# Performance work log

Hardware: AMD Instinct MI355X
Metric: run time of the kernel (lower is better)

Reference implementation:

```python
import jax, jax.numpy as jnp
import numpy as np

K = 3        # kernel_size
PAD = 1      # padding
STRIDE = 1   # stride (must be 1: module asserts offset HxW == input HxW)
DIL = 1      # dilation


def _bilinear_gather(x, py, px):
    """x: (B,C,H,W); py,px: (B,KK,Ho,Wo) float sample coords.
    Returns (B,C,KK,Ho,Wo), zero outside bounds (DCNv2 semantics)."""
    B, C, H, W = x.shape
    y0 = jnp.floor(py); x0 = jnp.floor(px)
    wy1 = py - y0; wy0 = 1.0 - wy1
    wx1 = px - x0; wx0 = 1.0 - wx1
    flat = x.reshape(B, C, H * W)

    def gather(yi, xi):
        valid = (yi >= 0) & (yi < H) & (xi >= 0) & (xi < W)
        yc = jnp.clip(yi, 0, H - 1).astype(jnp.int32)
        xc = jnp.clip(xi, 0, W - 1).astype(jnp.int32)
        idx = (yc * W + xc).reshape(B, 1, -1)                      # (B,1,KK*Ho*Wo)
        g = jnp.take_along_axis(flat, jnp.broadcast_to(idx, (B, C, idx.shape[-1])), axis=2)
        g = g.reshape(B, C, *yi.shape[1:])                          # (B,C,KK,Ho,Wo)
        return jnp.where(valid[:, None], g, 0.0)

    v00 = gather(y0, x0)
    v01 = gather(y0, x0 + 1)
    v10 = gather(y0 + 1, x0)
    v11 = gather(y0 + 1, x0 + 1)
    wy0 = wy0[:, None]; wy1 = wy1[:, None]; wx0 = wx0[:, None]; wx1 = wx1[:, None]
    return wy0 * (wx0 * v00 + wx1 * v01) + wy1 * (wx0 * v10 + wx1 * v11)


def dcn_v2(x, coord_offset, coord_weight, weight, bias):
    B, C, H, W = x.shape
    O = weight.shape[0]
    KK = K * K
    # offset channels ordered (k, [y,x]) per DCNv2 layout
    offs = coord_offset.reshape(B, KK, 2, H, W)
    oy, ox = offs[:, :, 0], offs[:, :, 1]
    ky, kx = jnp.meshgrid(jnp.arange(K), jnp.arange(K), indexing='ij')
    ky = ky.reshape(KK); kx = kx.reshape(KK)
    # base sampling grid for each output pixel / kernel tap: (KK,H,W)
    py = (jnp.arange(H) * STRIDE - PAD)[None, :, None] + (ky * DIL)[:, None, None]
    px = (jnp.arange(W) * STRIDE - PAD)[None, None, :] + (kx * DIL)[:, None, None]
    py = py.astype(x.dtype)[None] + oy   # (B,KK,H,W)
    px = px.astype(x.dtype)[None] + ox
    sampled = _bilinear_gather(x, py, px)              # (B,C,KK,H,W)
    sampled = sampled * coord_weight[:, None]          # modulation mask
    out = jnp.einsum('bckhw,ock->bohw', sampled, weight.reshape(O, C, KK))
    return out + bias[None, :, None, None]


def setup_inputs() -> dict:
    key = jax.random.key(0)
    k1, k2, k3, k4, k5 = jax.random.split(key, 5)
    B, C, O, H, W = 8, 256, 256, 64, 64
    return {
        'input': jax.random.normal(k1, (B, C, H, W), dtype=jnp.float32),
        'coord_offset': jax.random.normal(k2, (B, 2 * K * K, H, W), dtype=jnp.float32),
        'coord_weight': jax.random.uniform(k3, (B, K * K, H, W), dtype=jnp.float32),
        'weight': jax.random.normal(k4, (O, C, K, K), dtype=jnp.float32) * 0.02,
        'bias': jax.random.normal(k5, (O,), dtype=jnp.float32) * 0.01,
    }


def reference(input, coord_offset, coord_weight, weight, bias):
    return dcn_v2(input, coord_offset, coord_weight, weight, bias)
```

## Files before the change

### kernel.cpp

```cpp
#include <hip/hip_runtime.h>
#include <hip/hip_bf16.h>
#include <stdint.h>

typedef __bf16 bf16_t;
typedef bf16_t bf16x8 __attribute__((ext_vector_type(8)));
typedef float f32x4 __attribute__((ext_vector_type(4)));
typedef float f32x2 __attribute__((ext_vector_type(2)));

__global__ __launch_bounds__(256) void k_transpose(const float* __restrict__ x,
                                                   bf16_t* __restrict__ xt) {
    __shared__ __align__(16) bf16_t tile[256][66];
    const int b = blockIdx.x >> 6;
    const int y = blockIdx.x & 63;
    const int t = threadIdx.x;

    const float* src = x + ((size_t)(b * 256) * 64 + y) * 64;
    const int x4 = (t & 15) * 4;
    const int cs = t >> 4;
#pragma unroll
    for (int cc = 0; cc < 256; cc += 16) {
        int c = cc + cs;
        float4 v = *(const float4*)(src + (size_t)c * 4096 + x4);
        tile[c][x4 + 0] = (bf16_t)v.x;
        tile[c][x4 + 1] = (bf16_t)v.y;
        tile[c][x4 + 2] = (bf16_t)v.z;
        tile[c][x4 + 3] = (bf16_t)v.w;
    }
    __syncthreads();
    bf16_t* dst = xt + ((size_t)(b * 64 + y) * 64) * 256 + t;
#pragma unroll 8
    for (int xx = 0; xx < 64; ++xx) {
        dst[(size_t)xx * 256] = tile[t][xx];
    }
}

__global__ __launch_bounds__(256) void k_pack_w(const float* __restrict__ w,
                                                bf16_t* __restrict__ Wp) {
    const int kb2 = blockIdx.x;
    const int kk  = kb2 >> 2;
    const int cp  = kb2 & 3;
    const int o   = threadIdx.x;
    bf16_t* base = Wp + (size_t)kb2 * 16384 + o * 64;
#pragma unroll
    for (int j = 0; j < 8; ++j) {
        const int js = j ^ (o & 7);
        bf16x8 v;
#pragma unroll
        for (int e = 0; e < 8; ++e) {
            const int c = cp * 64 + j * 8 + e;
            v[e] = (bf16_t)w[(size_t)(o * 256 + c) * 9 + kk];
        }
        *(bf16x8*)(base + js * 8) = v;
    }
}

__global__ __launch_bounds__(512, 4) void k_dcn(
    const bf16_t* __restrict__ xt, const bf16_t* __restrict__ Wp,
    const float* __restrict__ coff, const float* __restrict__ cwm,
    const float* __restrict__ bias, float* __restrict__ out) {

    __shared__ __align__(16) bf16_t sW[256 * 64];
    __shared__ __align__(16) bf16_t sS[64 * 64];
    __shared__ float sCW[4][64];
    __shared__ int   sCA[4][64];

    const int blk = blockIdx.x;
    const int b  = blk & 7;
    const int h  = blk >> 3;
    const int t = threadIdx.x;
    const int wv = t >> 6;
    const int lane = t & 63;

    const int p = t >> 3;
    const int q = t & 7;

    const int fr = lane & 15;
    const int quad = lane >> 4;
    const int swz = fr & 7;

    f32x4 acc[2][4] = {};

    for (int kk = 0; kk < 9; ++kk) {
        if (t < 64) {
            const int wpx = t;
            float oy = coff[((size_t)(b * 18 + kk * 2 + 0) * 64 + h) * 64 + wpx];
            float ox = coff[((size_t)(b * 18 + kk * 2 + 1) * 64 + h) * 64 + wpx];
            float m  = cwm [((size_t)(b * 9 + kk) * 64 + h) * 64 + wpx];
            float py = (float)(h - 1 + (kk / 3)) + oy;
            float px = (float)(wpx - 1 + (kk % 3)) + ox;
            float fy = floorf(py), fx = floorf(px);
            int y0 = (int)fy, x0 = (int)fx;
            int y1 = y0 + 1,  x1 = x0 + 1;
            float wy1 = py - fy, wx1 = px - fx;
            float wy0 = 1.0f - wy1, wx0 = 1.0f - wx1;
            bool vy0 = (y0 >= 0) && (y0 < 64), vy1 = (y1 >= 0) && (y1 < 64);
            bool vx0 = (x0 >= 0) && (x0 < 64), vx1 = (x1 >= 0) && (x1 < 64);
            int yc0 = min(max(y0, 0), 63), yc1 = min(max(y1, 0), 63);
            int xc0 = min(max(x0, 0), 63), xc1 = min(max(x1, 0), 63);
            const int base = b * 4096;
            sCW[0][wpx] = (vy0 && vx0) ? wy0 * wx0 * m : 0.0f;
            sCW[1][wpx] = (vy0 && vx1) ? wy0 * wx1 * m : 0.0f;
            sCW[2][wpx] = (vy1 && vx0) ? wy1 * wx0 * m : 0.0f;
            sCW[3][wpx] = (vy1 && vx1) ? wy1 * wx1 * m : 0.0f;
            sCA[0][wpx] = (base + yc0 * 64 + xc0) * 256;
            sCA[1][wpx] = (base + yc0 * 64 + xc1) * 256;
            sCA[2][wpx] = (base + yc1 * 64 + xc0) * 256;
            sCA[3][wpx] = (base + yc1 * 64 + xc1) * 256;
        }
        __syncthreads();

        const float w0 = sCW[0][p], w1 = sCW[1][p];
        const float w2 = sCW[2][p], w3 = sCW[3][p];
        const bf16_t* c0 = xt + sCA[0][p] + q * 8;
        const bf16_t* c1 = xt + sCA[1][p] + q * 8;
        const bf16_t* c2 = xt + sCA[2][p] + q * 8;
        const bf16_t* c3 = xt + sCA[3][p] + q * 8;
        bf16_t* sSp = sS + p * 64 + ((q ^ (p & 7)) * 8);

        for (int cp = 0; cp < 4; ++cp) {
            {
                const char* g = ((const char*)Wp)
                              + ((size_t)(kk * 4 + cp)) * 32768 + t * 16;
                char* l = ((char*)sW) + t * 16;
#pragma unroll
                for (int i = 0; i < 4; ++i) {
                    __builtin_amdgcn_global_load_lds(
                        (const __attribute__((address_space(1))) unsigned int*)(g + i * 8192),
                        (__attribute__((address_space(3))) unsigned int*)(l + i * 8192),
                        16, 0, 0);
                }
            }
            {
                const int cb = cp * 64;
                f32x2 s2[4] = {};
                {
                    bf16x8 v = *(const bf16x8*)(c0 + cb);
                    f32x2 ww = {w0, w0};
#pragma unroll
                    for (int j = 0; j < 4; ++j) { f32x2 f = {(float)v[2 * j], (float)v[2 * j + 1]}; s2[j] += ww * f; }
                }
                {
                    bf16x8 v = *(const bf16x8*)(c1 + cb);
                    f32x2 ww = {w1, w1};
#pragma unroll
                    for (int j = 0; j < 4; ++j) { f32x2 f = {(float)v[2 * j], (float)v[2 * j + 1]}; s2[j] += ww * f; }
                }
                {
                    bf16x8 v = *(const bf16x8*)(c2 + cb);
                    f32x2 ww = {w2, w2};
#pragma unroll
                    for (int j = 0; j < 4; ++j) { f32x2 f = {(float)v[2 * j], (float)v[2 * j + 1]}; s2[j] += ww * f; }
                }
                {
                    bf16x8 v = *(const bf16x8*)(c3 + cb);
                    f32x2 ww = {w3, w3};
#pragma unroll
                    for (int j = 0; j < 4; ++j) { f32x2 f = {(float)v[2 * j], (float)v[2 * j + 1]}; s2[j] += ww * f; }
                }
                bf16x8 ov;
#pragma unroll
                for (int j = 0; j < 4; ++j) {
                    ov[2 * j]     = (bf16_t)s2[j][0];
                    ov[2 * j + 1] = (bf16_t)s2[j][1];
                }
                *(bf16x8*)sSp = ov;
            }
            __syncthreads();

#pragma unroll
            for (int s = 0; s < 2; ++s) {
                const int cidx = s * 4 + quad;
                const int coff_e = (cidx ^ swz) * 8;
                bf16x8 a[2], bb[4];
#pragma unroll
                for (int mt = 0; mt < 2; ++mt)
                    a[mt] = *(const bf16x8*)(sW + (wv * 32 + mt * 16 + fr) * 64 + coff_e);
#pragma unroll
                for (int nt = 0; nt < 4; ++nt)
                    bb[nt] = *(const bf16x8*)(sS + (nt * 16 + fr) * 64 + coff_e);
#pragma unroll
                for (int mt = 0; mt < 2; ++mt)
#pragma unroll
                    for (int nt = 0; nt < 4; ++nt)
                        acc[mt][nt] = __builtin_amdgcn_mfma_f32_16x16x32_bf16(
                            a[mt], bb[nt], acc[mt][nt], 0, 0, 0);
            }
            __syncthreads();
        }
    }

    const int rowq = quad * 4;
#pragma unroll
    for (int mt = 0; mt < 2; ++mt) {
#pragma unroll
        for (int r = 0; r < 4; ++r) {
            const int og = wv * 32 + mt * 16 + rowq + r;
            const float bs = bias[og];
            float* op = out + ((size_t)(b * 256 + og) * 64 + h) * 64;
#pragma unroll
            for (int nt = 0; nt < 4; ++nt) {
                op[nt * 16 + fr] = acc[mt][nt][r] + bs;
            }
        }
    }
}

extern "C" void kernel_launch(void* const* d_in, const int* in_sizes, int n_in,
                              void* d_out, int out_size, void* d_ws, size_t ws_size,
                              hipStream_t stream) {
    const float* x    = (const float*)d_in[0];
    const float* coff = (const float*)d_in[1];
    const float* cwm  = (const float*)d_in[2];
    const float* wgt  = (const float*)d_in[3];
    const float* bias = (const float*)d_in[4];
    float* out = (float*)d_out;

    bf16_t* xt = (bf16_t*)d_ws;
    bf16_t* Wp = xt + (size_t)8 * 64 * 64 * 256;

    k_transpose<<<512, 256, 0, stream>>>(x, xt);
    k_pack_w   <<<36,  256, 0, stream>>>(wgt, Wp);
    k_dcn      <<<512, 512, 0, stream>>>(xt, Wp, coff, cwm, bias, out);
}
```

Before: 165.1 us.

## Double-buffer sampled tile, load weights directly to registers, precompute all tap coords

The main kernel now precomputes bilinear coordinates and weights for all nine taps once, instead of recomputing them per tap with separate barriers. Weights move from an LDS staging buffer to direct global-to-register loads in an MFMA-ready layout, prefetched one iteration ahead. The sampled tile is double-buffered so gathering the next chunk overlaps the current MFMAs, which halves the barriers per iteration. The transpose and weight-pack kernels are rewritten to do vectorized, coalesced stores through LDS. The cost is more register use for the prefetched A fragments and more LDS for the coordinate tables.

New measurement: 153.9 us. 1.07x faster.

```diff
diff --git a/kernel.cpp b/kernel.cpp
--- a/kernel.cpp
+++ b/kernel.cpp
@@ -9,7 +9,7 @@
 
 __global__ __launch_bounds__(256) void k_transpose(const float* __restrict__ x,
                                                    bf16_t* __restrict__ xt) {
-    __shared__ __align__(16) bf16_t tile[256][66];
+    __shared__ __align__(16) bf16_t tT[64][264];
     const int b = blockIdx.x >> 6;
     const int y = blockIdx.x & 63;
     const int t = threadIdx.x;
@@ -21,36 +21,46 @@
     for (int cc = 0; cc < 256; cc += 16) {
         int c = cc + cs;
         float4 v = *(const float4*)(src + (size_t)c * 4096 + x4);
-        tile[c][x4 + 0] = (bf16_t)v.x;
-        tile[c][x4 + 1] = (bf16_t)v.y;
-        tile[c][x4 + 2] = (bf16_t)v.z;
-        tile[c][x4 + 3] = (bf16_t)v.w;
-    }
-    __syncthreads();
-    bf16_t* dst = xt + ((size_t)(b * 64 + y) * 64) * 256 + t;
-#pragma unroll 8
-    for (int xx = 0; xx < 64; ++xx) {
-        dst[(size_t)xx * 256] = tile[t][xx];
+        tT[x4 + 0][c] = (bf16_t)v.x;
+        tT[x4 + 1][c] = (bf16_t)v.y;
+        tT[x4 + 2][c] = (bf16_t)v.z;
+        tT[x4 + 3][c] = (bf16_t)v.w;
+    }
+    __syncthreads();
+    bf16_t* dst = xt + ((size_t)(b * 64 + y) * 64) * 256;
+#pragma unroll
+    for (int i = 0; i < 8; ++i) {
+        const int s = t + 256 * i;
+        const int xx = s >> 5, cg = s & 31;
+        *(bf16x8*)(dst + xx * 256 + cg * 8) = *(const bf16x8*)&tT[xx][cg * 8];
     }
 }
 
 __global__ __launch_bounds__(256) void k_pack_w(const float* __restrict__ w,
                                                 bf16_t* __restrict__ Wp) {
-    const int kb2 = blockIdx.x;
-    const int kk  = kb2 >> 2;
-    const int cp  = kb2 & 3;
-    const int o   = threadIdx.x;
-    bf16_t* base = Wp + (size_t)kb2 * 16384 + o * 64;
-#pragma unroll
-    for (int j = 0; j < 8; ++j) {
-        const int js = j ^ (o & 7);
+    __shared__ float lw[8 * 2304];
+    const int t = threadIdx.x;
+    const int o0 = blockIdx.x * 8;
+    const float4* src = (const float4*)(w + (size_t)o0 * 2304);
+#pragma unroll
+    for (int i = 0; i < 18; ++i) {
+        ((float4*)lw)[t + 256 * i] = src[t + 256 * i];
+    }
+    __syncthreads();
+#pragma unroll
+    for (int i = 0; i < 9; ++i) {
+        const int u = t + 256 * i;
+        const int o = u / 288, r = u - o * 288;
+        const int kb2 = r >> 3, rr = r & 7;
+        const int s = rr >> 2, qq = rr & 3;
+        const int kk = kb2 >> 2, cp = kb2 & 3;
         bf16x8 v;
 #pragma unroll
         for (int e = 0; e < 8; ++e) {
-            const int c = cp * 64 + j * 8 + e;
-            v[e] = (bf16_t)w[(size_t)(o * 256 + c) * 9 + kk];
-        }
-        *(bf16x8*)(base + js * 8) = v;
+            const int c = cp * 64 + s * 32 + qq * 8 + e;
+            v[e] = (bf16_t)lw[o * 2304 + c * 9 + kk];
+        }
+        *(bf16x8*)(Wp + ((size_t)(kb2 * 2 + s) * 256 + o0 + o) * 32 + qq * 8) = v;
     }
 }
 
@@ -59,10 +69,9 @@
     const float* __restrict__ coff, const float* __restrict__ cwm,
     const float* __restrict__ bias, float* __restrict__ out) {
 
-    __shared__ __align__(16) bf16_t sW[256 * 64];
-    __shared__ __align__(16) bf16_t sS[64 * 64];
-    __shared__ float sCW[4][64];
-    __shared__ int   sCA[4][64];
+    __shared__ __align__(16) bf16_t sS[2][64 * 64];
+    __shared__ float sCW[9][4][64];
+    __shared__ int   sCA[9][4][64];
 
     const int blk = blockIdx.x;
     const int b  = blk & 7;
@@ -78,115 +87,111 @@
     const int quad = lane >> 4;
     const int swz = fr & 7;
 
+    for (int u = t; u < 576; u += 512) {
+        const int kk = u >> 6, wpx = u & 63;
+        float oy = coff[((size_t)(b * 18 + kk * 2 + 0) * 64 + h) * 64 + wpx];
+        float ox = coff[((size_t)(b * 18 + kk * 2 + 1) * 64 + h) * 64 + wpx];
+        float m  = cwm [((size_t)(b * 9 + kk) * 64 + h) * 64 + wpx];
+        float py = (float)(h - 1 + (kk / 3)) + oy;
+        float px = (float)(wpx - 1 + (kk % 3)) + ox;
+        float fy = floorf(py), fx = floorf(px);
+        int y0 = (int)fy, x0 = (int)fx;
+        int y1 = y0 + 1,  x1 = x0 + 1;
+        float wy1 = py - fy, wx1 = px - fx;
+        float wy0 = 1.0f - wy1, wx0 = 1.0f - wx1;
+        bool vy0 = (y0 >= 0) && (y0 < 64), vy1 = (y1 >= 0) && (y1 < 64);
+        bool vx0 = (x0 >= 0) && (x0 < 64), vx1 = (x1 >= 0) && (x1 < 64);
+        int yc0 = min(max(y0, 0), 63), yc1 = min(max(y1, 0), 63);
+        int xc0 = min(max(x0, 0), 63), xc1 = min(max(x1, 0), 63);
+        const int base = b * 4096;
+        sCW[kk][0][wpx] = (vy0 && vx0) ? wy0 * wx0 * m : 0.0f;
+        sCW[kk][1][wpx] = (vy0 && vx1) ? wy0 * wx1 * m : 0.0f;
+        sCW[kk][2][wpx] = (vy1 && vx0) ? wy1 * wx0 * m : 0.0f;
+        sCW[kk][3][wpx] = (vy1 && vx1) ? wy1 * wx1 * m : 0.0f;
+        sCA[kk][0][wpx] = (base + yc0 * 64 + xc0) * 256;
+        sCA[kk][1][wpx] = (base + yc0 * 64 + xc1) * 256;
+        sCA[kk][2][wpx] = (base + yc1 * 64 + xc0) * 256;
+        sCA[kk][3][wpx] = (base + yc1 * 64 + xc1) * 256;
+    }
+    __syncthreads();
+
+    const bf16_t* wA = Wp + (wv * 32 + fr) * 32 + quad * 8;
+    bf16_t* sSw0 = &sS[0][0] + p * 64 + ((q ^ (p & 7)) * 8);
+
     f32x4 acc[2][4] = {};
-
-    for (int kk = 0; kk < 9; ++kk) {
-        if (t < 64) {
-            const int wpx = t;
-            float oy = coff[((size_t)(b * 18 + kk * 2 + 0) * 64 + h) * 64 + wpx];
-            float ox = coff[((size_t)(b * 18 + kk * 2 + 1) * 64 + h) * 64 + wpx];
-            float m  = cwm [((size_t)(b * 9 + kk) * 64 + h) * 64 + wpx];
-            float py = (float)(h - 1 + (kk / 3)) + oy;
-            float px = (float)(wpx - 1 + (kk % 3)) + ox;
-            float fy = floorf(py), fx = floorf(px);
-            int y0 = (int)fy, x0 = (int)fx;
-            int y1 = y0 + 1,  x1 = x0 + 1;
-            float wy1 = py - fy, wx1 = px - fx;
-            float wy0 = 1.0f - wy1, wx0 = 1.0f - wx1;
-            bool vy0 = (y0 >= 0) && (y0 < 64), vy1 = (y1 >= 0) && (y1 < 64);
-            bool vx0 = (x0 >= 0) && (x0 < 64), vx1 = (x1 >= 0) && (x1 < 64);
-            int yc0 = min(max(y0, 0), 63), yc1 = min(max(y1, 0), 63);
-            int xc0 = min(max(x0, 0), 63), xc1 = min(max(x1, 0), 63);
-            const int base = b * 4096;
-            sCW[0][wpx] = (vy0 && vx0) ? wy0 * wx0 * m : 0.0f;
-            sCW[1][wpx] = (vy0 && vx1) ? wy0 * wx1 * m : 0.0f;
-            sCW[2][wpx] = (vy1 && vx0) ? wy1 * wx0 * m : 0.0f;
-            sCW[3][wpx] = (vy1 && vx1) ? wy1 * wx1 * m : 0.0f;
-            sCA[0][wpx] = (base + yc0 * 64 + xc0) * 256;
-            sCA[1][wpx] = (base + yc0 * 64 + xc1) * 256;
-            sCA[2][wpx] = (base + yc1 * 64 + xc0) * 256;
-            sCA[3][wpx] = (base + yc1 * 64 + xc1) * 256;
+    bf16x8 aC[2][2], aN[2][2];
+
+    auto sample_into = [&](int iter, int buf) {
+        const int kk = iter >> 2, cp = iter & 3;
+        const float w0 = sCW[kk][0][p], w1 = sCW[kk][1][p];
+        const float w2 = sCW[kk][2][p], w3 = sCW[kk][3][p];
+        const int cb = cp * 64 + q * 8;
+        bf16x8 g0 = *(const bf16x8*)(xt + sCA[kk][0][p] + cb);
+        bf16x8 g1 = *(const bf16x8*)(xt + sCA[kk][1][p] + cb);
+        bf16x8 g2 = *(const bf16x8*)(xt + sCA[kk][2][p] + cb);
+        bf16x8 g3 = *(const bf16x8*)(xt + sCA[kk][3][p] + cb);
+        f32x2 s2[4] = {};
+        f32x2 W0 = {w0, w0}, W1 = {w1, w1}, W2 = {w2, w2}, W3 = {w3, w3};
+#pragma unroll
+        for (int j = 0; j < 4; ++j) {
+            f32x2 f0 = {(float)g0[2 * j], (float)g0[2 * j + 1]};
+            f32x2 f1 = {(float)g1[2 * j], (float)g1[2 * j + 1]};
+            f32x2 f2 = {(float)g2[2 * j], (float)g2[2 * j + 1]};
+            f32x2 f3 = {(float)g3[2 * j], (float)g3[2 * j + 1]};
+            s2[j] += W0 * f0; s2[j] += W1 * f1; s2[j] += W2 * f2; s2[j] += W3 * f3;
+        }
+        bf16x8 ov;
+#pragma unroll
+        for (int j = 0; j < 4; ++j) {
+            ov[2 * j]     = (bf16_t)s2[j][0];
+            ov[2 * j + 1] = (bf16_t)s2[j][1];
+        }
+        *(bf16x8*)(sSw0 + buf * 4096) = ov;
+    };
+
+    auto do_mfma = [&](int cur) {
+        const bf16_t* sb = &sS[cur][0];
+#pragma unroll
+        for (int s = 0; s < 2; ++s) {
+            const int coffe = ((s * 4 + quad) ^ swz) * 8;
+            bf16x8 bb[4];
+#pragma unroll
+            for (int nt = 0; nt < 4; ++nt)
+                bb[nt] = *(const bf16x8*)(sb + (nt * 16 + fr) * 64 + coffe);
+#pragma unroll
+            for (int mt = 0; mt < 2; ++mt)
+#pragma unroll
+                for (int nt = 0; nt < 4; ++nt)
+                    acc[mt][nt] = __builtin_amdgcn_mfma_f32_16x16x32_bf16(
+                        aC[mt][s], bb[nt], acc[mt][nt], 0, 0, 0);
+        }
+    };
+
+    sample_into(0, 0);
+    aC[0][0] = *(const bf16x8*)(wA);
+    aC[0][1] = *(const bf16x8*)(wA + 8192);
+    aC[1][0] = *(const bf16x8*)(wA + 512);
+    aC[1][1] = *(const bf16x8*)(wA + 8192 + 512);
+    __syncthreads();
+
+    for (int iter = 0; iter < 36; ++iter) {
+        const int cur = iter & 1;
+        if (iter < 35) {
+            const bf16_t* wn = wA + (size_t)(iter + 1) * 16384;
+            aN[0][0] = *(const bf16x8*)(wn);
+            aN[0][1] = *(const bf16x8*)(wn + 8192);
+            aN[1][0] = *(const bf16x8*)(wn + 512);
+            aN[1][1] = *(const bf16x8*)(wn + 8192 + 512);
+            sample_into(iter + 1, 1 - cur);
+            do_mfma(cur);
+#pragma unroll
+            for (int mt = 0; mt < 2; ++mt)
+#pragma unroll
+                for (int s = 0; s < 2; ++s) aC[mt][s] = aN[mt][s];
+        } else {
+            do_mfma(cur);
         }
         __syncthreads();
-
-        const float w0 = sCW[0][p], w1 = sCW[1][p];
-        const float w2 = sCW[2][p], w3 = sCW[3][p];
-        const bf16_t* c0 = xt + sCA[0][p] + q * 8;
-        const bf16_t* c1 = xt + sCA[1][p] + q * 8;
-        const bf16_t* c2 = xt + sCA[2][p] + q * 8;
-        const bf16_t* c3 = xt + sCA[3][p] + q * 8;
-        bf16_t* sSp = sS + p * 64 + ((q ^ (p & 7)) * 8);
-
-        for (int cp = 0; cp < 4; ++cp) {
-            {
-                const char* g = ((const char*)Wp)
-                              + ((size_t)(kk * 4 + cp)) * 32768 + t * 16;
-                char* l = ((char*)sW) + t * 16;
-#pragma unroll
-                for (int i = 0; i < 4; ++i) {
-                    __builtin_amdgcn_global_load_lds(
-                        (const __attribute__((address_space(1))) unsigned int*)(g + i * 8192),
-                        (__attribute__((address_space(3))) unsigned int*)(l + i * 8192),
-                        16, 0, 0);
-                }
-            }
-            {
-                const int cb = cp * 64;
-                f32x2 s2[4] = {};
-                {
-                    bf16x8 v = *(const bf16x8*)(c0 + cb);
-                    f32x2 ww = {w0, w0};
-#pragma unroll
-                    for (int j = 0; j < 4; ++j) { f32x2 f = {(float)v[2 * j], (float)v[2 * j + 1]}; s2[j] += ww * f; }
-                }
-                {
-                    bf16x8 v = *(const bf16x8*)(c1 + cb);
-                    f32x2 ww = {w1, w1};
-#pragma unroll
-                    for (int j = 0; j < 4; ++j) { f32x2 f = {(float)v[2 * j], (float)v[2 * j + 1]}; s2[j] += ww * f; }
-                }
-                {
-                    bf16x8 v = *(const bf16x8*)(c2 + cb);
-                    f32x2 ww = {w2, w2};
-#pragma unroll
-                    for (int j = 0; j < 4; ++j) { f32x2 f = {(float)v[2 * j], (float)v[2 * j + 1]}; s2[j] += ww * f; }
-                }
-                {
-                    bf16x8 v = *(const bf16x8*)(c3 + cb);
-                    f32x2 ww = {w3, w3};
-#pragma unroll
-                    for (int j = 0; j < 4; ++j) { f32x2 f = {(float)v[2 * j], (float)v[2 * j + 1]}; s2[j] += ww * f; }
-                }
-                bf16x8 ov;
-#pragma unroll
-                for (int j = 0; j < 4; ++j) {
-                    ov[2 * j]     = (bf16_t)s2[j][0];
-                    ov[2 * j + 1] = (bf16_t)s2[j][1];
-                }
-                *(bf16x8*)sSp = ov;
-            }
-            __syncthreads();
-
-#pragma unroll
-            for (int s = 0; s < 2; ++s) {
-                const int cidx = s * 4 + quad;
-                const int coff_e = (cidx ^ swz) * 8;
-                bf16x8 a[2], bb[4];
-#pragma unroll
-                for (int mt = 0; mt < 2; ++mt)
-                    a[mt] = *(const bf16x8*)(sW + (wv * 32 + mt * 16 + fr) * 64 + coff_e);
-#pragma unroll
-                for (int nt = 0; nt < 4; ++nt)
-                    bb[nt] = *(const bf16x8*)(sS + (nt * 16 + fr) * 64 + coff_e);
-#pragma unroll
-                for (int mt = 0; mt < 2; ++mt)
-#pragma unroll
-                    for (int nt = 0; nt < 4; ++nt)
-                        acc[mt][nt] = __builtin_amdgcn_mfma_f32_16x16x32_bf16(
-                            a[mt], bb[nt], acc[mt][nt], 0, 0, 0);
-            }
-            __syncthreads();
-        }
     }
 
     const int rowq = quad * 4;
@@ -219,6 +224,6 @@
     bf16_t* Wp = xt + (size_t)8 * 64 * 64 * 256;
 
     k_transpose<<<512, 256, 0, stream>>>(x, xt);
-    k_pack_w   <<<36,  256, 0, stream>>>(wgt, Wp);
+    k_pack_w   <<<32,  256, 0, stream>>>(wgt, Wp);
     k_dcn      <<<512, 512, 0, stream>>>(xt, Wp, coff, cwm, bias, out);
 }
```
